# Performance work log

Hardware: AMD Instinct MI355X
Metric: run time of the kernel (lower is better)

## Reference

```python
import jax, jax.numpy as jnp
import numpy as np

DIM = 512
CHUNK = 64
DEPTH = 2
LR = 0.1
MOM = 0.9
DEC = 0.01
EPS_RMS = 1.1920929e-07  # torch.finfo(float32).eps, RMSNorm default
EPS_L2 = 1e-12           # F.normalize default eps


def rmsnorm(x, g):
    return x * jax.lax.rsqrt(jnp.mean(x * x, axis=-1, keepdims=True) + EPS_RMS) * g


def l2norm(x):
    n = jnp.sqrt(jnp.sum(x * x, axis=-1, keepdims=True))
    return x / jnp.maximum(n, EPS_L2)


def mlp(ws, x):
    # MemoryMLP: Linear(no bias) stack with SiLU between layers
    h = x
    for i, W in enumerate(ws):
        h = h @ W.T
        if i < len(ws) - 1:
            h = jax.nn.silu(h)
    return h


def setup_inputs() -> dict:
    key = jax.random.key(0)
    ks = jax.random.split(key, 16)
    D = DIM
    xav = np.sqrt(6.0 / (D + D)).astype(np.float32)  # xavier_uniform for square Linear
    inp = {
        'x': jax.random.normal(ks[0], (4, 4096, D), jnp.float32),
        'M': jax.random.normal(ks[1], (4, D, D), jnp.float32),
        'mem_W': 0.02 * jax.random.normal(ks[2], (DEPTH, D, D), jnp.float32),
        'Wk': jax.random.uniform(ks[3], (D, D), jnp.float32, -xav, xav),
        'Wv': jax.random.uniform(ks[4], (D, D), jnp.float32, -xav, xav),
        'Wq': jax.random.uniform(ks[5], (D, D), jnp.float32, -xav, xav),
        'Wout': jax.random.uniform(ks[6], (D, D), jnp.float32, -xav, xav),
        'Wgd': jax.random.uniform(ks[7], (D, D), jnp.float32, -1/np.sqrt(D), 1/np.sqrt(D)),
        'bgd': jax.random.uniform(ks[8], (D,), jnp.float32, -1/np.sqrt(D), 1/np.sqrt(D)),
        'Wgl': jax.random.uniform(ks[9], (D, D), jnp.float32, -1/np.sqrt(D), 1/np.sqrt(D)),
        'bgl': jax.random.uniform(ks[10], (D,), jnp.float32, -1/np.sqrt(D), 1/np.sqrt(D)),
        'Wgm': jax.random.uniform(ks[11], (D, D), jnp.float32, -1/np.sqrt(D), 1/np.sqrt(D)),
        'bgm': jax.random.uniform(ks[12], (D,), jnp.float32, -1/np.sqrt(D), 1/np.sqrt(D)),
        'gs': jnp.ones((D,), jnp.float32),
        'gr': jnp.ones((D,), jnp.float32),
    }
    return inp


def reference(x, M, mem_W, Wk, Wv, Wq, Wout, Wgd, bgd, Wgl, bgl, Wgm, bgm, gs, gr):
    B, S, D = x.shape
    pad = (CHUNK - S % CHUNK) % CHUNK
    if pad > 0:
        x = jnp.pad(x, ((0, 0), (0, pad), (0, 0)))
    Sp = x.shape[1]
    n = Sp // CHUNK

    # data-dependent gates from chunk means, batch-averaged scalars per chunk
    cm = x.reshape(B, n, CHUNK, D).mean(axis=2)                      # [B,n,D]
    alpha = (jax.nn.sigmoid(cm @ Wgd.T + bgd).mean(-1) * DEC).mean(0)  # [n]
    theta = (jax.nn.sigmoid(cm @ Wgl.T + bgl).mean(-1) * LR).mean(0)   # [n]
    eta = (jax.nn.sigmoid(cm @ Wgm.T + bgm).mean(-1) * MOM).mean(0)    # [n]

    x_store = rmsnorm(x, gs)
    k = l2norm(jax.nn.silu(jnp.einsum('bsd,bde->bse', x_store, M) @ Wk.T))
    v = jax.nn.silu(x_store @ Wv.T)
    q = l2norm(jax.nn.silu(rmsnorm(x, gr) @ Wq.T))

    # [n, B, C, D] chunked, scan over chunk axis
    def chunked(t):
        return t.reshape(B, n, CHUNK, D).transpose(1, 0, 2, 3)
    qc, kc, vc = chunked(q), chunked(k), chunked(v)

    ws0 = tuple(mem_W[i] for i in range(DEPTH))
    mom0 = tuple(jnp.zeros_like(w) for w in ws0)

    def step(carry, xs):
        ws, mom = carry
        q_t, k_t, v_t, a, th, et = xs
        retrieved = mlp(ws, q_t)                                   # retrieve with pre-update weights
        loss_fn = lambda w: jnp.mean((mlp(w, k_t) - v_t) ** 2)      # Eq. 12
        grads = jax.grad(loss_fn)(ws)
        mom = jax.tree.map(lambda m, g: et * m - th * g, mom, grads)   # Eq. 14
        ws = jax.tree.map(lambda w, s: (1.0 - a) * w + s, ws, mom)     # Eq. 13
        return (ws, mom), retrieved

    _, retrieved = jax.lax.scan(step, (ws0, mom0), (qc, kc, vc, alpha, theta, eta))
    retrieved = retrieved.transpose(1, 0, 2, 3).reshape(B, Sp, D)[:, :S]
    return retrieved @ Wout.T
```

## Files before the change

kernel.cpp:

```cpp
#include <hip/hip_runtime.h>
#include <math.h>
#include <stdint.h>

#define D512 512
#define SC_E (2.0f / 131072.0f)

typedef __attribute__((ext_vector_type(8))) __bf16 bf16x8;
typedef __attribute__((ext_vector_type(4))) float f32x4;
#define MFMA(a,b,c) __builtin_amdgcn_mfma_f32_16x16x32_bf16(a,b,c,0,0,0)

__device__ __forceinline__ float sigmoidf_(float z){ return 1.0f/(1.0f+expf(-z)); }
__device__ __forceinline__ float siluf_(float z){ return z/(1.0f+expf(-z)); }
__device__ __forceinline__ float dsiluf_(float z){ float s=1.0f/(1.0f+expf(-z)); return s*(1.0f+z*(1.0f-s)); }

__device__ __forceinline__ unsigned short f2bf(float x){
  union { float f; unsigned u; } c; c.f = x;
  unsigned r = (c.u + 0x7fffu + ((c.u >> 16) & 1u)) >> 16;
  return (unsigned short)r;
}
__device__ __forceinline__ float bf2f(unsigned short s){
  union { unsigned u; float f; } c; c.u = ((unsigned)s) << 16; return c.f;
}
__device__ __forceinline__ void split2(float x, unsigned short& h, unsigned short& l){
  h = f2bf(x); l = f2bf(x - bf2f(h));
}
__device__ __forceinline__ bf16x8 ldf(const unsigned short* p){ return *(const bf16x8*)p; }

__device__ __forceinline__ void stc_u32(unsigned* p, unsigned v){
  __hip_atomic_store(p, v, __ATOMIC_RELAXED, __HIP_MEMORY_SCOPE_AGENT);
}
__device__ __forceinline__ void stc_u64(unsigned long long* p, unsigned long long v){
  __hip_atomic_store(p, v, __ATOMIC_RELAXED, __HIP_MEMORY_SCOPE_AGENT);
}
__device__ __forceinline__ void stc_us4(unsigned short* p, ushort4 v){
  union { ushort4 s; unsigned long long q; } u; u.s = v;
  stc_u64((unsigned long long*)p, u.q);
}
__device__ __forceinline__ void stc_pair(unsigned short* p, unsigned short v){
  unsigned ov = (unsigned)__shfl_xor((int)(unsigned)v, 1, 64);
  if (!(threadIdx.x & 1))
    stc_u32((unsigned*)p, ((unsigned)v) | (ov << 16));
}

__device__ __forceinline__ void gbar_h(unsigned* bar, int grp, bool leader, unsigned p){
  __syncthreads();
  if (threadIdx.x == 0){
    unsigned* cnt = bar + grp*64;
    unsigned* go  = bar + 512 + grp*64;
    unsigned* gl  = bar + 1024;
    __hip_atomic_fetch_add(cnt, 1u, __ATOMIC_RELAXED, __HIP_MEMORY_SCOPE_AGENT);
    if (leader){
      while (__hip_atomic_load(cnt, __ATOMIC_RELAXED, __HIP_MEMORY_SCOPE_AGENT) < 32u*p)
        __builtin_amdgcn_s_sleep(1);
      __hip_atomic_fetch_add(gl, 1u, __ATOMIC_RELAXED, __HIP_MEMORY_SCOPE_AGENT);
      while (__hip_atomic_load(gl, __ATOMIC_RELAXED, __HIP_MEMORY_SCOPE_AGENT) < 8u*p)
        __builtin_amdgcn_s_sleep(1);
      __hip_atomic_store(go, p, __ATOMIC_RELAXED, __HIP_MEMORY_SCOPE_AGENT);
    } else {
      while (__hip_atomic_load(go, __ATOMIC_RELAXED, __HIP_MEMORY_SCOPE_AGENT) < p)
        __builtin_amdgcn_s_sleep(2);
    }
  }
  __syncthreads();
  __atomic_signal_fence(__ATOMIC_ACQUIRE);
}

template<int KTOT>
__device__ __forceinline__ void tile_ss(const unsigned short* __restrict__ A, int lda,
                                        const unsigned short* __restrict__ B, int ldb,
                                        f32x4* acc){
  const int lane = threadIdx.x & 63, wave = threadIdx.x >> 6;
  const int kq = (lane >> 4) << 3;
  const size_t aoff = (size_t)(wave*16 + (lane & 15)) * lda + kq;
  const size_t boff0 = (size_t)(lane & 15) * ldb + kq;
#pragma unroll
  for (int k0 = 0; k0 < KTOT; k0 += 32){
    bf16x8 av = ldf(A + aoff + k0);
#pragma unroll
    for (int nn = 0; nn < 4; nn++){
      bf16x8 bv = ldf(B + boff0 + (size_t)(nn*16)*ldb + k0);
      acc[nn] = MFMA(av, bv, acc[nn]);
    }
  }
}

template<int KTOT>
__device__ __forceinline__ void tile_dd(const unsigned short* __restrict__ Ah, const unsigned short* __restrict__ Al, int lda,
                                        const unsigned short* __restrict__ Bh, const unsigned short* __restrict__ Bl, int ldb,
                                        f32x4* acc){
  const int lane = threadIdx.x & 63, wave = threadIdx.x >> 6;
  const int kq = (lane >> 4) << 3;
  const size_t aoff = (size_t)(wave*16 + (lane & 15)) * lda + kq;
  const size_t boff0 = (size_t)(lane & 15) * ldb + kq;
#pragma unroll
  for (int k0 = 0; k0 < KTOT; k0 += 32){
    bf16x8 ah = ldf(Ah + aoff + k0);
    bf16x8 al = ldf(Al + aoff + k0);
#pragma unroll
    for (int nn = 0; nn < 4; nn++){
      const size_t bo = boff0 + (size_t)(nn*16)*ldb + k0;
      bf16x8 bh = ldf(Bh + bo);
      bf16x8 bl = ldf(Bl + bo);
      acc[nn] = MFMA(ah, bh, acc[nn]);
      acc[nn] = MFMA(ah, bl, acc[nn]);
      acc[nn] = MFMA(al, bh, acc[nn]);
    }
  }
}

template<int KTOT>
__device__ __forceinline__ void slice_ss(const unsigned short* __restrict__ A16, int lda,
                                         const unsigned short* __restrict__ B64, int ldb,
                                         f32x4& acc){
  const int lane = threadIdx.x & 63, wave = threadIdx.x >> 6;
  const int kq = (lane >> 4) << 3;
  const size_t aoff = (size_t)(lane & 15) * lda + kq;
  const size_t boff = (size_t)(wave*16 + (lane & 15)) * ldb + kq;
#pragma unroll
  for (int k0 = 0; k0 < KTOT; k0 += 32){
    bf16x8 av = ldf(A16 + aoff + k0);
    bf16x8 bv = ldf(B64 + boff + k0);
    acc = MFMA(av, bv, acc);
  }
}

template<int KTOT>
__device__ __forceinline__ void slice_dd(const unsigned short* __restrict__ Ah, const unsigned short* __restrict__ Al, int lda,
                                         const unsigned short* __restrict__ Bh, const unsigned short* __restrict__ Bl, int ldb,
                                         f32x4& acc){
  const int lane = threadIdx.x & 63, wave = threadIdx.x >> 6;
  const int kq = (lane >> 4) << 3;
  const size_t aoff = (size_t)(lane & 15) * lda + kq;
  const size_t boff = (size_t)(wave*16 + (lane & 15)) * ldb + kq;
#pragma unroll
  for (int k0 = 0; k0 < KTOT; k0 += 32){
    bf16x8 ah = ldf(Ah + aoff + k0);
    bf16x8 al = ldf(Al + aoff + k0);
    bf16x8 bh = ldf(Bh + boff + k0);
    bf16x8 bl = ldf(Bl + boff + k0);
    acc = MFMA(ah, bh, acc);
    acc = MFMA(ah, bl, acc);
    acc = MFMA(al, bh, acc);
  }
}

__global__ void rms_store_kernel(const float* __restrict__ x, const float* __restrict__ g,
                                 unsigned short* __restrict__ dstH){
  const size_t row = blockIdx.x; const int tid = threadIdx.x;
  const float4 xv = *(const float4*)(x + row * D512 + tid * 4);
  float ss = xv.x*xv.x + xv.y*xv.y + xv.z*xv.z + xv.w*xv.w;
  for (int o = 32; o > 0; o >>= 1) ss += __shfl_xor(ss, o, 64);
  __shared__ float w2[2];
  if ((tid & 63) == 0) w2[tid >> 6] = ss;
  __syncthreads();
  const float r = rsqrtf((w2[0] + w2[1]) * (1.0f / 512.0f) + 1.1920929e-07f);
  const float4 gv = *(const float4*)(g + tid * 4);
  ushort4 h;
  h.x = f2bf(xv.x*r*gv.x); h.y = f2bf(xv.y*r*gv.y); h.z = f2bf(xv.z*r*gv.z); h.w = f2bf(xv.w*r*gv.w);
  *(ushort4*)(dstH + row * D512 + tid * 4) = h;
}

__global__ void rms_retr_kernel(const float* __restrict__ x, const float* __restrict__ g,
                                unsigned short* __restrict__ dstH, unsigned short* __restrict__ dstL){
  const size_t row = blockIdx.x; const int tid = threadIdx.x;
  const float4 xv = *(const float4*)(x + row * D512 + tid * 4);
  float ss = xv.x*xv.x + xv.y*xv.y + xv.z*xv.z + xv.w*xv.w;
  for (int o = 32; o > 0; o >>= 1) ss += __shfl_xor(ss, o, 64);
  __shared__ float w2[2];
  if ((tid & 63) == 0) w2[tid >> 6] = ss;
  __syncthreads();
  const float r = rsqrtf((w2[0] + w2[1]) * (1.0f / 512.0f) + 1.1920929e-07f);
  const float4 gv = *(const float4*)(g + tid * 4);
  float v0 = xv.x*r*gv.x, v1 = xv.y*r*gv.y, v2 = xv.z*r*gv.z, v3 = xv.w*r*gv.w;
  ushort4 h, l;
  split2(v0, h.x, l.x); split2(v1, h.y, l.y); split2(v2, h.z, l.z); split2(v3, h.w, l.w);
  *(ushort4*)(dstH + row * D512 + tid * 4) = h;
  *(ushort4*)(dstL + row * D512 + tid * 4) = l;
}

__global__ void l2norm_split_kernel(float* __restrict__ buf,
                                    unsigned short* __restrict__ dstH, unsigned short* __restrict__ dstL){
  const size_t row = blockIdx.x; const int tid = threadIdx.x;
  float4 xv = *(const float4*)(buf + row * D512 + tid * 4);
  float ss = xv.x*xv.x + xv.y*xv.y + xv.z*xv.z + xv.w*xv.w;
  for (int o = 32; o > 0; o >>= 1) ss += __shfl_xor(ss, o, 64);
  __shared__ float w2[2];
  if ((tid & 63) == 0) w2[tid >> 6] = ss;
  __syncthreads();
  const float n = sqrtf(w2[0] + w2[1]);
  const float sc = 1.0f / fmaxf(n, 1e-12f);
  xv.x *= sc; xv.y *= sc; xv.z *= sc; xv.w *= sc;
  *(float4*)(buf + row * D512 + tid * 4) = xv;
  ushort4 h; h.x = f2bf(xv.x); h.y = f2bf(xv.y); h.z = f2bf(xv.z); h.w = f2bf(xv.w);
  *(ushort4*)(dstH + row * D512 + tid * 4) = h;
  if (dstL){
    ushort4 l;
    l.x = f2bf(xv.x - bf2f(h.x)); l.y = f2bf(xv.y - bf2f(h.y));
    l.z = f2bf(xv.z - bf2f(h.z)); l.w = f2bf(xv.w - bf2f(h.w));
    *(ushort4*)(dstL + row * D512 + tid * 4) = l;
  }
}

__global__ void cast_kernel(const float* __restrict__ src, unsigned short* __restrict__ dstH,
                            unsigned short* __restrict__ dstL, int n){
  int i = (blockIdx.x * 256 + threadIdx.x) * 4;
  if (i >= n) return;
  float4 v = *(const float4*)(src + i);
  ushort4 h; h.x = f2bf(v.x); h.y = f2bf(v.y); h.z = f2bf(v.z); h.w = f2bf(v.w);
  *(ushort4*)(dstH + i) = h;
  if (dstL){
    ushort4 l;
    l.x = f2bf(v.x - bf2f(h.x)); l.y = f2bf(v.y - bf2f(h.y));
    l.z = f2bf(v.z - bf2f(h.z)); l.w = f2bf(v.w - bf2f(h.w));
    *(ushort4*)(dstL + i) = l;
  }
}

__global__ void trans_cast_kernel(const float* __restrict__ src, unsigned short* __restrict__ dstH,
                                  unsigned short* __restrict__ dstL, int R, int C,
                                  size_t sbs, size_t dbs){
  __shared__ float t[64][65];
  const int b = blockIdx.z;
  const float* s = src + (size_t)b * sbs;
  const int r0 = blockIdx.y * 64, c0 = blockIdx.x * 64;
  for (int i = threadIdx.x; i < 4096; i += 256){
    int rr = i >> 6, cc = i & 63;
    t[rr][cc] = s[(size_t)(r0 + rr) * C + c0 + cc];
  }
  __syncthreads();
  for (int i = threadIdx.x; i < 4096; i += 256){
    int cc = i >> 6, rr = i & 63;
    float v = t[rr][cc];
    size_t off = (size_t)b * dbs + (size_t)(c0 + cc) * R + r0 + rr;
    unsigned short h = f2bf(v);
    dstH[off] = h;
    if (dstL) dstL[off] = f2bf(v - bf2f(h));
  }
}

__global__ void chunk_mean_kernel(const float* __restrict__ x, float* __restrict__ cm){
  const int c = blockIdx.x, b = blockIdx.y, tid = threadIdx.x;
  const float* base = x + ((size_t)b * 4096 + (size_t)c * 64) * D512 + tid * 4;
  float4 s = {0,0,0,0};
  for (int r = 0; r < 64; r++){
    const float4 v = *(const float4*)(base + (size_t)r * D512);
    s.x += v.x; s.y += v.y; s.z += v.z; s.w += v.w;
  }
  const float inv = 1.0f / 64.0f;
  s.x *= inv; s.y *= inv; s.z *= inv; s.w *= inv;
  *(float4*)(cm + ((size_t)b * 64 + c) * D512 + tid * 4) = s;
}

__global__ void gates_kernel(const float* __restrict__ cm,
                             const float* __restrict__ Wgd, const float* __restrict__ bgd,
                             const float* __restrict__ Wgl, const float* __restrict__ bgl,
                             const float* __restrict__ Wgm, const float* __restrict__ bgm,
                             float* __restrict__ alpha, float* __restrict__ theta, float* __restrict__ eta){
  const int c = blockIdx.x, tid = threadIdx.x;
  __shared__ float cmsh[512];
  float s0 = 0.f, s1 = 0.f, s2 = 0.f;
  for (int b = 0; b < 4; b++){
    __syncthreads();
    if (tid < 128){
      const float4 v = *(const float4*)(cm + ((size_t)b * 64 + c) * D512 + tid * 4);
      *(float4*)&cmsh[tid * 4] = v;
    }
    __syncthreads();
    for (int j = tid; j < 512; j += 256){
      float d0 = bgd[j], d1 = bgl[j], d2 = bgm[j];
      const float* w0 = Wgd + (size_t)j * D512;
      const float* w1 = Wgl + (size_t)j * D512;
      const float* w2 = Wgm + (size_t)j * D512;
      for (int kk = 0; kk < 512; kk += 4){
        const float4 cv = *(const float4*)&cmsh[kk];
        const float4 a = *(const float4*)(w0 + kk); d0 += cv.x*a.x + cv.y*a.y + cv.z*a.z + cv.w*a.w;
        const float4 e = *(const float4*)(w1 + kk); d1 += cv.x*e.x + cv.y*e.y + cv.z*e.z + cv.w*e.w;
        const float4 g = *(const float4*)(w2 + kk); d2 += cv.x*g.x + cv.y*g.y + cv.z*g.z + cv.w*g.w;
      }
      s0 += sigmoidf_(d0); s1 += sigmoidf_(d1); s2 += sigmoidf_(d2);
    }
  }
  __shared__ float red[256];
  const float inv = 1.0f / 2048.0f;
  red[tid] = s0; __syncthreads();
  for (int o = 128; o > 0; o >>= 1){ if (tid < o) red[tid] += red[tid + o]; __syncthreads(); }
  if (tid == 0) alpha[c] = red[0] * inv * 0.01f;
  __syncthreads();
  red[tid] = s1; __syncthreads();
  for (int o = 128; o > 0; o >>= 1){ if (tid < o) red[tid] += red[tid + o]; __syncthreads(); }
  if (tid == 0) theta[c] = red[0] * inv * 0.1f;
  __syncthreads();
  red[tid] = s2; __syncthreads();
  for (int o = 128; o > 0; o >>= 1){ if (tid < o) red[tid] += red[tid + o]; __syncthreads(); }
  if (tid == 0) eta[c] = red[0] * inv * 0.9f;
}

template<int MODE>
__global__ __launch_bounds__(256) void gemm_ss(const unsigned short* __restrict__ A,
                                               const unsigned short* __restrict__ B, size_t bzs,
                                               void* __restrict__ out){
  const int lane = threadIdx.x & 63, wave = threadIdx.x >> 6;
  const int er = wave*16 + ((lane >> 4) << 2), ec = lane & 15;
  const size_t row0 = (size_t)blockIdx.z * 4096 + (size_t)blockIdx.x * 64;
  const int n0 = blockIdx.y * 64;
  f32x4 acc[4] = {};
  tile_ss<512>(A + row0 * D512, D512, B + (size_t)blockIdx.z * bzs + (size_t)n0 * D512, D512, acc);
#pragma unroll
  for (int nn = 0; nn < 4; nn++)
#pragma unroll
    for (int r = 0; r < 4; r++){
      const size_t off = (row0 + er + r) * D512 + n0 + nn*16 + ec;
      float val = acc[nn][r];
      if (MODE == 0) ((unsigned short*)out)[off] = f2bf(val);
      else if (MODE == 1) ((float*)out)[off] = siluf_(val);
      else ((float*)out)[off] = val;
    }
}

template<int MODE>
__global__ __launch_bounds__(256) void gemm_dd(const unsigned short* __restrict__ Ah, const unsigned short* __restrict__ Al,
                                               const unsigned short* __restrict__ Bh, const unsigned short* __restrict__ Bl,
                                               float* __restrict__ out){
  const int lane = threadIdx.x & 63, wave = threadIdx.x >> 6;
  const int er = wave*16 + ((lane >> 4) << 2), ec = lane & 15;
  const size_t row0 = (size_t)blockIdx.x * 64;
  const int n0 = blockIdx.y * 64;
  f32x4 acc[4] = {};
  tile_dd<512>(Ah + row0 * D512, Al + row0 * D512, D512,
               Bh + (size_t)n0 * D512, Bl + (size_t)n0 * D512, D512, acc);
#pragma unroll
  for (int nn = 0; nn < 4; nn++)
#pragma unroll
    for (int r = 0; r < 4; r++){
      const size_t off = (row0 + er + r) * D512 + n0 + nn*16 + ec;
      out[off] = (MODE == 1) ? siluf_(acc[nn][r]) : acc[nn][r];
    }
}

struct ScanArgs {
  const unsigned short* kbH;
  const unsigned short* qbH; const unsigned short* qbL;
  unsigned short* W0bH; unsigned short* W0bL;
  unsigned short* hkbH; unsigned short* hkTbH;
  unsigned short* hqbH; unsigned short* hqbL;
  unsigned short* W1bH; unsigned short* W1bL;
  const float* v;
  unsigned short* ebH; unsigned short* eTbH;
  unsigned short* retH; unsigned short* retL;
  unsigned short* W1TbH; unsigned short* dpTbH;
  const float* alpha; const float* theta; const float* eta;
  const unsigned short* kTbH;
  const float* W0f; const float* W1f;
  unsigned* bar;
};

__global__ __launch_bounds__(256, 2) void scan_fused(ScanArgs P){
  const int bid = blockIdx.x;
  const int s = bid >> 6;
  const int T = bid & 63;
  const int grp = bid & 7;
  const bool leader = (bid < 8);
  const int lane = threadIdx.x & 63, wave = threadIdx.x >> 6;
  const int ar = (lane >> 4) << 2;
  const int bc = wave*16 + (lane & 15);
  const int kq = (lane >> 4) << 3;

  const int jx = T >> 3, dx = T & 7;
  f32x4 w0r = {}, m0r = {}, w1r = {}, m1r = {};
  const size_t woff = (size_t)(jx*64 + s*16 + ar) * D512 + dx*64 + bc;
#pragma unroll
  for (int r = 0; r < 4; r++){
    w0r[r] = P.W0f[woff + (size_t)r * D512];
    w1r[r] = P.W1f[woff + (size_t)r * D512];
  }

  unsigned p = 0;
  for (int t = 0; t < 64; ++t){
    float4 sp = {0,0,0,0};

    if (T < 32){
      const int ib = T >> 3, jxa = T & 7;
      f32x4 acc = {};
      slice_ss<512>(P.kbH + ((size_t)ib*4096 + (size_t)t*64 + s*16) * D512, D512,
                    P.W0bH + (size_t)jxa*64 * D512, D512, acc);
      const int i0 = ib*64 + s*16 + ar;
      const int j  = jxa*64 + bc;
      ushort4 hv;
#pragma unroll
      for (int r = 0; r < 4; r++){
        const float pfull = acc[r];
        const unsigned short hb = f2bf(siluf_(pfull));
        stc_pair(&P.hkbH[(size_t)(i0 + r) * D512 + j], hb);
        ((unsigned short*)&hv)[r] = hb;
        ((float*)&sp)[r] = dsiluf_(pfull);
      }
      stc_us4(&P.hkTbH[(size_t)j * 256 + i0], hv);
    } else {
      const int u = T - 32, bt = u >> 3, nx = u & 7;
      const size_t ab = ((size_t)bt*4096 + (size_t)t*64 + s*16) * D512;
      f32x4 acc = {};
      slice_dd<512>(P.qbH + ab, P.qbL + ab, D512,
                    P.W0bH + (size_t)nx*64 * D512, P.W0bL + (size_t)nx*64 * D512, D512, acc);
      const int i0 = bt*64 + s*16 + ar;
      const int j  = nx*64 + bc;
#pragma unroll
      for (int r = 0; r < 4; r++){
        const float h = siluf_(acc[r]);
        unsigned short hh, ll; split2(h, hh, ll);
        stc_pair(&P.hqbH[(size_t)(i0 + r) * D512 + j], hh);
        stc_pair(&P.hqbL[(size_t)(i0 + r) * D512 + j], ll);
      }
    }
    ++p; gbar_h(P.bar, grp, leader, p);

    if (T < 32){
      const int ib = T >> 3, nx = T & 7;
      f32x4 acc = {};
      slice_ss<512>(P.hkbH + (size_t)(ib*64 + s*16) * D512, D512,
                    P.W1bH + (size_t)nx*64 * D512, D512, acc);
      const int i0 = ib*64 + s*16 + ar;
      const int m  = nx*64 + bc;
      ushort4 ev;
#pragma unroll
      for (int r = 0; r < 4; r++){
        const size_t grow = (size_t)ib*4096 + (size_t)t*64 + s*16 + ar + r;
        const float vv = P.v[grow * D512 + m];
        const unsigned short eb = f2bf((acc[r] - vv) * SC_E);
        stc_pair(&P.ebH[(size_t)(i0 + r) * D512 + m], eb);
        ((unsigned short*)&ev)[r] = eb;
      }
      stc_us4(&P.eTbH[(size_t)m * 256 + i0], ev);
    } else {
      const int u = T - 32, bt = u >> 3, nx = u & 7;
      const size_t ab = (size_t)(bt*64 + s*16) * D512;
      f32x4 acc = {};
      slice_dd<512>(P.hqbH + ab, P.hqbL + ab, D512,
                    P.W1bH + (size_t)nx*64 * D512, P.W1bL + (size_t)nx*64 * D512, D512, acc);
#pragma unroll
      for (int r = 0; r < 4; r++){
        const size_t grow = (size_t)bt*4096 + (size_t)t*64 + s*16 + ar + r;
        unsigned short hh, ll; split2(acc[r], hh, ll);
        const size_t off = grow * D512 + nx*64 + bc;
        P.retH[off] = hh; P.retL[off] = ll;
      }
    }
    ++p; gbar_h(P.bar, grp, leader, p);

    if (T < 32){
      const int ib = T >> 3, jxa = T & 7;
      f32x4 acc = {};
      slice_ss<512>(P.ebH + (size_t)(ib*64 + s*16) * D512, D512,
                    P.W1TbH + (size_t)jxa*64 * D512, D512, acc);
      const int i0 = ib*64 + s*16 + ar;
      const int j  = jxa*64 + bc;
      ushort4 dv;
#pragma unroll
      for (int r = 0; r < 4; r++)
        ((unsigned short*)&dv)[r] = f2bf(acc[r] * ((const float*)&sp)[r]);
      stc_us4(&P.dpTbH[(size_t)j * 256 + i0], dv);
    }
    ++p; gbar_h(P.bar, grp, leader, p);

    {
      f32x4 g0 = {};
      const unsigned short* A16 = P.dpTbH + (size_t)(jx*64 + s*16) * 256;
      const size_t aoff = (size_t)(lane & 15) * 256 + kq;
      const size_t brow = (size_t)(dx*64 + bc) * 4096;
#pragma unroll
      for (int k0 = 0; k0 < 256; k0 += 32){
        bf16x8 av = ldf(A16 + aoff + k0);
        const int pl = k0 >> 6;
        bf16x8 bv = ldf(P.kTbH + (size_t)pl * (512*4096) + brow + (size_t)t*64 + (k0 & 63) + kq);
        g0 = MFMA(av, bv, g0);
      }
      f32x4 g1 = {};
      slice_ss<256>(P.eTbH + (size_t)(jx*64 + s*16) * 256, 256,
                    P.hkTbH + (size_t)(dx*64) * 256, 256, g1);
      const float al = P.alpha[t], th = P.theta[t], et = P.eta[t];
      ushort4 tv;
#pragma unroll
      for (int r = 0; r < 4; r++){
        const size_t off = woff + (size_t)r * D512;
        m0r[r] = et * m0r[r] - th * g0[r];
        w0r[r] = (1.0f - al) * w0r[r] + m0r[r];
        unsigned short hh, ll; split2(w0r[r], hh, ll);
        stc_pair(&P.W0bH[off], hh); stc_pair(&P.W0bL[off], ll);
        m1r[r] = et * m1r[r] - th * g1[r];
        w1r[r] = (1.0f - al) * w1r[r] + m1r[r];
        unsigned short h1, l1; split2(w1r[r], h1, l1);
        stc_pair(&P.W1bH[off], h1); stc_pair(&P.W1bL[off], l1);
        ((unsigned short*)&tv)[r] = h1;
      }
      stc_us4(&P.W1TbH[(size_t)(dx*64 + bc) * D512 + jx*64 + s*16 + ar], tv);
    }
    ++p; gbar_h(P.bar, grp, leader, p);

    __builtin_amdgcn_fence(__ATOMIC_ACQUIRE, "agent");
  }
}

extern "C" void kernel_launch(void* const* d_in, const int* in_sizes, int n_in,
                              void* d_out, int out_size, void* d_ws, size_t ws_size,
                              hipStream_t stream) {
  const float* x    = (const float*)d_in[0];
  const float* Mb   = (const float*)d_in[1];
  const float* memW = (const float*)d_in[2];
  const float* Wk   = (const float*)d_in[3];
  const float* Wv   = (const float*)d_in[4];
  const float* Wq   = (const float*)d_in[5];
  const float* Wout = (const float*)d_in[6];
  const float* Wgd  = (const float*)d_in[7];
  const float* bgd  = (const float*)d_in[8];
  const float* Wgl  = (const float*)d_in[9];
  const float* bgl  = (const float*)d_in[10];
  const float* Wgm  = (const float*)d_in[11];
  const float* bgm  = (const float*)d_in[12];
  const float* gs   = (const float*)d_in[13];
  const float* gr   = (const float*)d_in[14];
  float* out = (float*)d_out;

  const size_t NBIG = (size_t)4 * 4096 * 512;
  char* p = (char*)d_ws;
  auto alloc_f = [&](size_t n) -> float* {
    p = (char*)(((uintptr_t)p + 255) & ~(uintptr_t)255);
    float* r = (float*)p; p += n * 4; return r;
  };
  auto alloc_s = [&](size_t n) -> unsigned short* {
    p = (char*)(((uintptr_t)p + 255) & ~(uintptr_t)255);
    unsigned short* r = (unsigned short*)p; p += n * 2; return r;
  };

  float* v       = alloc_f(NBIG);
  float* scratch = alloc_f(NBIG);
  float* W0f     = alloc_f(262144);
  float* W1f     = alloc_f(262144);
  float* cm      = alloc_f(131072);
  float* alpha   = alloc_f(64);
  float* theta   = alloc_f(64);
  float* eta     = alloc_f(64);
  unsigned* bar  = (unsigned*)alloc_f(2048);

  unsigned short* xsbH = alloc_s(NBIG);
  unsigned short* xmbH = alloc_s(NBIG);
  unsigned short* xrbL = alloc_s(NBIG);
  unsigned short* qbH  = alloc_s(NBIG);
  unsigned short* qbL  = alloc_s(NBIG);
  unsigned short* kbH  = alloc_s(NBIG);
  unsigned short* kTbH = alloc_s(NBIG);
  unsigned short* W0bH = alloc_s(262144);
  unsigned short* W0bL = alloc_s(262144);
  unsigned short* W1bH = alloc_s(262144);
  unsigned short* W1bL = alloc_s(262144);
  unsigned short* W1TbH = alloc_s(262144);
  unsigned short* WkbH = alloc_s(262144);
  unsigned short* WvbH = alloc_s(262144);
  unsigned short* WqbH = alloc_s(262144);
  unsigned short* WqbL = alloc_s(262144);
  unsigned short* WoutbH = alloc_s(262144);
  unsigned short* WoutbL = alloc_s(262144);
  unsigned short* MTbH = alloc_s((size_t)4 * 262144);
  unsigned short* hkbH = alloc_s(131072);
  unsigned short* hkTbH = alloc_s(131072);
  unsigned short* hqbH = alloc_s(131072);
  unsigned short* hqbL = alloc_s(131072);
  unsigned short* ebH  = alloc_s(131072);
  unsigned short* eTbH = alloc_s(131072);
  unsigned short* dpTbH = alloc_s(131072);

  hipMemcpyAsync(W0f, memW, 2 * 262144 * sizeof(float), hipMemcpyDeviceToDevice, stream);
  hipMemsetAsync(bar, 0, 2048 * sizeof(unsigned), stream);
  cast_kernel<<<256, 256, 0, stream>>>(memW, W0bH, W0bL, 262144);
  cast_kernel<<<256, 256, 0, stream>>>(memW + 262144, W1bH, W1bL, 262144);
  trans_cast_kernel<<<dim3(8, 8, 1), 256, 0, stream>>>(memW + 262144, W1TbH, nullptr, 512, 512, 0, 0);
  cast_kernel<<<256, 256, 0, stream>>>(Wk, WkbH, nullptr, 262144);
  cast_kernel<<<256, 256, 0, stream>>>(Wv, WvbH, nullptr, 262144);
  cast_kernel<<<256, 256, 0, stream>>>(Wq, WqbH, WqbL, 262144);
  cast_kernel<<<256, 256, 0, stream>>>(Wout, WoutbH, WoutbL, 262144);
  trans_cast_kernel<<<dim3(8, 8, 4), 256, 0, stream>>>(Mb, MTbH, nullptr, 512, 512, 262144, 262144);

  rms_store_kernel<<<16384, 128, 0, stream>>>(x, gs, xsbH);
  chunk_mean_kernel<<<dim3(64, 4), 128, 0, stream>>>(x, cm);
  gates_kernel<<<64, 256, 0, stream>>>(cm, Wgd, bgd, Wgl, bgl, Wgm, bgm, alpha, theta, eta);

  gemm_ss<0><<<dim3(64, 8, 4), 256, 0, stream>>>(xsbH, MTbH, 262144, xmbH);
  gemm_ss<1><<<dim3(256, 8, 1), 256, 0, stream>>>(xmbH, WkbH, 0, scratch);
  l2norm_split_kernel<<<16384, 128, 0, stream>>>(scratch, kbH, nullptr);
  trans_cast_kernel<<<dim3(8, 64, 4), 256, 0, stream>>>(scratch, kTbH, nullptr, 4096, 512, 2097152, 2097152);
  gemm_ss<1><<<dim3(256, 8, 1), 256, 0, stream>>>(xsbH, WvbH, 0, v);
  rms_retr_kernel<<<16384, 128, 0, stream>>>(x, gr, xmbH, xrbL);
  gemm_dd<1><<<dim3(256, 8), 256, 0, stream>>>(xmbH, xrbL, WqbH, WqbL, scratch);
  l2norm_split_kernel<<<16384, 128, 0, stream>>>(scratch, qbH, qbL);

  unsigned short* retH = xsbH;
  unsigned short* retL = xmbH;

  ScanArgs sa;
  sa.kbH = kbH; sa.qbH = qbH; sa.qbL = qbL;
  sa.W0bH = W0bH; sa.W0bL = W0bL;
  sa.hkbH = hkbH; sa.hkTbH = hkTbH;
  sa.hqbH = hqbH; sa.hqbL = hqbL;
  sa.W1bH = W1bH; sa.W1bL = W1bL;
  sa.v = v;
  sa.ebH = ebH; sa.eTbH = eTbH;
  sa.retH = retH; sa.retL = retL;
  sa.W1TbH = W1TbH; sa.dpTbH = dpTbH;
  sa.alpha = alpha; sa.theta = theta; sa.eta = eta;
  sa.kTbH = kTbH;
  sa.W0f = W0f; sa.W1f = W1f;
  sa.bar = bar;
  scan_fused<<<256, 256, 0, stream>>>(sa);

  gemm_dd<2><<<dim3(256, 8), 256, 0, stream>>>(retH, retL, WoutbH, WoutbL, out);
}
```

Before: 3.591 ms.

## Split scan GEMM K-dimension across two wave halves and batch gate dot products

The persistent scan kernel now launches 512 threads per block. Two wave groups each compute half of the K reduction for every slice GEMM and combine the partial sums through shared memory, and the two weight-gradient GEMMs in the update phase are assigned to separate wave halves. This shortens the serial MFMA chain per wave on the latency-bound chunk scan, at the cost of extra __syncthreads, LDS traffic and lower occupancy per CU. Separately, the gates kernel loads all four batch chunk-means at once and reuses each weight row load across the four batches.

```diff
diff --git a/kernel.cpp b/kernel.cpp
--- a/kernel.cpp
+++ b/kernel.cpp
@@ -111,11 +111,11 @@
 template<int KTOT>
 __device__ __forceinline__ void slice_ss(const unsigned short* __restrict__ A16, int lda,
                                          const unsigned short* __restrict__ B64, int ldb,
-                                         f32x4& acc){
-  const int lane = threadIdx.x & 63, wave = threadIdx.x >> 6;
-  const int kq = (lane >> 4) << 3;
+                                         f32x4& acc, int koff){
+  const int lane = threadIdx.x & 63, w4 = (threadIdx.x >> 6) & 3;
+  const int kq = ((lane >> 4) << 3) + koff;
   const size_t aoff = (size_t)(lane & 15) * lda + kq;
-  const size_t boff = (size_t)(wave*16 + (lane & 15)) * ldb + kq;
+  const size_t boff = (size_t)(w4*16 + (lane & 15)) * ldb + kq;
 #pragma unroll
   for (int k0 = 0; k0 < KTOT; k0 += 32){
     bf16x8 av = ldf(A16 + aoff + k0);
@@ -127,11 +127,11 @@
 template<int KTOT>
 __device__ __forceinline__ void slice_dd(const unsigned short* __restrict__ Ah, const unsigned short* __restrict__ Al, int lda,
                                          const unsigned short* __restrict__ Bh, const unsigned short* __restrict__ Bl, int ldb,
-                                         f32x4& acc){
-  const int lane = threadIdx.x & 63, wave = threadIdx.x >> 6;
-  const int kq = (lane >> 4) << 3;
+                                         f32x4& acc, int koff){
+  const int lane = threadIdx.x & 63, w4 = (threadIdx.x >> 6) & 3;
+  const int kq = ((lane >> 4) << 3) + koff;
   const size_t aoff = (size_t)(lane & 15) * lda + kq;
-  const size_t boff = (size_t)(wave*16 + (lane & 15)) * ldb + kq;
+  const size_t boff = (size_t)(w4*16 + (lane & 15)) * ldb + kq;
 #pragma unroll
   for (int k0 = 0; k0 < KTOT; k0 += 32){
     bf16x8 ah = ldf(Ah + aoff + k0);
@@ -257,27 +257,35 @@
                              const float* __restrict__ Wgm, const float* __restrict__ bgm,
                              float* __restrict__ alpha, float* __restrict__ theta, float* __restrict__ eta){
   const int c = blockIdx.x, tid = threadIdx.x;
-  __shared__ float cmsh[512];
+  __shared__ float cmsh[4][512];
+#pragma unroll
+  for (int b = 0; b < 4; b++)
+    if (tid < 128)
+      *(float4*)&cmsh[b][tid * 4] = *(const float4*)(cm + ((size_t)b * 64 + c) * D512 + tid * 4);
+  __syncthreads();
   float s0 = 0.f, s1 = 0.f, s2 = 0.f;
-  for (int b = 0; b < 4; b++){
-    __syncthreads();
-    if (tid < 128){
-      const float4 v = *(const float4*)(cm + ((size_t)b * 64 + c) * D512 + tid * 4);
-      *(float4*)&cmsh[tid * 4] = v;
-    }
-    __syncthreads();
-    for (int j = tid; j < 512; j += 256){
-      float d0 = bgd[j], d1 = bgl[j], d2 = bgm[j];
-      const float* w0 = Wgd + (size_t)j * D512;
-      const float* w1 = Wgl + (size_t)j * D512;
-      const float* w2 = Wgm + (size_t)j * D512;
-      for (int kk = 0; kk < 512; kk += 4){
-        const float4 cv = *(const float4*)&cmsh[kk];
-        const float4 a = *(const float4*)(w0 + kk); d0 += cv.x*a.x + cv.y*a.y + cv.z*a.z + cv.w*a.w;
-        const float4 e = *(const float4*)(w1 + kk); d1 += cv.x*e.x + cv.y*e.y + cv.z*e.z + cv.w*e.w;
-        const float4 g = *(const float4*)(w2 + kk); d2 += cv.x*g.x + cv.y*g.y + cv.z*g.z + cv.w*g.w;
-      }
-      s0 += sigmoidf_(d0); s1 += sigmoidf_(d1); s2 += sigmoidf_(d2);
+  for (int j = tid; j < 512; j += 256){
+    float d0[4], d1[4], d2[4];
+#pragma unroll
+    for (int b = 0; b < 4; b++){ d0[b] = bgd[j]; d1[b] = bgl[j]; d2[b] = bgm[j]; }
+    const float* w0 = Wgd + (size_t)j * D512;
+    const float* w1 = Wgl + (size_t)j * D512;
+    const float* w2 = Wgm + (size_t)j * D512;
+    for (int kk = 0; kk < 512; kk += 4){
+      const float4 a = *(const float4*)(w0 + kk);
+      const float4 e = *(const float4*)(w1 + kk);
+      const float4 g = *(const float4*)(w2 + kk);
+#pragma unroll
+      for (int b = 0; b < 4; b++){
+        const float4 cv = *(const float4*)&cmsh[b][kk];
+        d0[b] += cv.x*a.x + cv.y*a.y + cv.z*a.z + cv.w*a.w;
+        d1[b] += cv.x*e.x + cv.y*e.y + cv.z*e.z + cv.w*e.w;
+        d2[b] += cv.x*g.x + cv.y*g.y + cv.z*g.z + cv.w*g.w;
+      }
+    }
+#pragma unroll
+    for (int b = 0; b < 4; b++){
+      s0 += sigmoidf_(d0[b]); s1 += sigmoidf_(d1[b]); s2 += sigmoidf_(d2[b]);
     }
   }
   __shared__ float red[256];
@@ -354,24 +362,33 @@
   unsigned* bar;
 };
 
-__global__ __launch_bounds__(256, 2) void scan_fused(ScanArgs P){
+__global__ __launch_bounds__(512, 1) void scan_fused(ScanArgs P){
   const int bid = blockIdx.x;
   const int s = bid >> 6;
   const int T = bid & 63;
   const int grp = bid & 7;
   const bool leader = (bid < 8);
-  const int lane = threadIdx.x & 63, wave = threadIdx.x >> 6;
+  const int tid = threadIdx.x;
+  const int lane = tid & 63;
+  const int wave = tid >> 6;
+  const int w4 = wave & 3;
+  const int h = wave >> 2;
   const int ar = (lane >> 4) << 2;
-  const int bc = wave*16 + (lane & 15);
+  const int bc = w4*16 + (lane & 15);
   const int kq = (lane >> 4) << 3;
+  const int koff = h * 256;
+
+  __shared__ f32x4 red[4][64];
 
   const int jx = T >> 3, dx = T & 7;
   f32x4 w0r = {}, m0r = {}, w1r = {}, m1r = {};
   const size_t woff = (size_t)(jx*64 + s*16 + ar) * D512 + dx*64 + bc;
-#pragma unroll
-  for (int r = 0; r < 4; r++){
-    w0r[r] = P.W0f[woff + (size_t)r * D512];
-    w1r[r] = P.W1f[woff + (size_t)r * D512];
+  if (h == 0){
+#pragma unroll
+    for (int r = 0; r < 4; r++){
+      w0r[r] = P.W0f[woff + (size_t)r * D512];
+      w1r[r] = P.W1f[woff + (size_t)r * D512];
+    }
   }
 
   unsigned p = 0;
@@ -381,34 +398,44 @@
     if (T < 32){
       const int ib = T >> 3, jxa = T & 7;
       f32x4 acc = {};
-      slice_ss<512>(P.kbH + ((size_t)ib*4096 + (size_t)t*64 + s*16) * D512, D512,
-                    P.W0bH + (size_t)jxa*64 * D512, D512, acc);
-      const int i0 = ib*64 + s*16 + ar;
-      const int j  = jxa*64 + bc;
-      ushort4 hv;
-#pragma unroll
-      for (int r = 0; r < 4; r++){
-        const float pfull = acc[r];
-        const unsigned short hb = f2bf(siluf_(pfull));
-        stc_pair(&P.hkbH[(size_t)(i0 + r) * D512 + j], hb);
-        ((unsigned short*)&hv)[r] = hb;
-        ((float*)&sp)[r] = dsiluf_(pfull);
-      }
-      stc_us4(&P.hkTbH[(size_t)j * 256 + i0], hv);
+      slice_ss<256>(P.kbH + ((size_t)ib*4096 + (size_t)t*64 + s*16) * D512, D512,
+                    P.W0bH + (size_t)jxa*64 * D512, D512, acc, koff);
+      if (h == 1) red[w4][lane] = acc;
+      __syncthreads();
+      if (h == 0){
+        const f32x4 o = red[w4][lane];
+        const int i0 = ib*64 + s*16 + ar;
+        const int j  = jxa*64 + bc;
+        ushort4 hv;
+#pragma unroll
+        for (int r = 0; r < 4; r++){
+          const float pfull = acc[r] + o[r];
+          const unsigned short hb = f2bf(siluf_(pfull));
+          stc_pair(&P.hkbH[(size_t)(i0 + r) * D512 + j], hb);
+          ((unsigned short*)&hv)[r] = hb;
+          ((float*)&sp)[r] = dsiluf_(pfull);
+        }
+        stc_us4(&P.hkTbH[(size_t)j * 256 + i0], hv);
+      }
     } else {
       const int u = T - 32, bt = u >> 3, nx = u & 7;
       const size_t ab = ((size_t)bt*4096 + (size_t)t*64 + s*16) * D512;
       f32x4 acc = {};
-      slice_dd<512>(P.qbH + ab, P.qbL + ab, D512,
-                    P.W0bH + (size_t)nx*64 * D512, P.W0bL + (size_t)nx*64 * D512, D512, acc);
-      const int i0 = bt*64 + s*16 + ar;
-      const int j  = nx*64 + bc;
-#pragma unroll
-      for (int r = 0; r < 4; r++){
-        const float h = siluf_(acc[r]);
-        unsigned short hh, ll; split2(h, hh, ll);
-        stc_pair(&P.hqbH[(size_t)(i0 + r) * D512 + j], hh);
-        stc_pair(&P.hqbL[(size_t)(i0 + r) * D512 + j], ll);
+      slice_dd<256>(P.qbH + ab, P.qbL + ab, D512,
+                    P.W0bH + (size_t)nx*64 * D512, P.W0bL + (size_t)nx*64 * D512, D512, acc, koff);
+      if (h == 1) red[w4][lane] = acc;
+      __syncthreads();
+      if (h == 0){
+        const f32x4 o = red[w4][lane];
+        const int i0 = bt*64 + s*16 + ar;
+        const int j  = nx*64 + bc;
+#pragma unroll
+        for (int r = 0; r < 4; r++){
+          const float hq = siluf_(acc[r] + o[r]);
+          unsigned short hh, ll; split2(hq, hh, ll);
+          stc_pair(&P.hqbH[(size_t)(i0 + r) * D512 + j], hh);
+          stc_pair(&P.hqbL[(size_t)(i0 + r) * D512 + j], ll);
+        }
       }
     }
     ++p; gbar_h(P.bar, grp, leader, p);
@@ -416,32 +443,42 @@
     if (T < 32){
       const int ib = T >> 3, nx = T & 7;
       f32x4 acc = {};
-      slice_ss<512>(P.hkbH + (size_t)(ib*64 + s*16) * D512, D512,
-                    P.W1bH + (size_t)nx*64 * D512, D512, acc);
-      const int i0 = ib*64 + s*16 + ar;
-      const int m  = nx*64 + bc;
-      ushort4 ev;
-#pragma unroll
-      for (int r = 0; r < 4; r++){
-        const size_t grow = (size_t)ib*4096 + (size_t)t*64 + s*16 + ar + r;
-        const float vv = P.v[grow * D512 + m];
-        const unsigned short eb = f2bf((acc[r] - vv) * SC_E);
-        stc_pair(&P.ebH[(size_t)(i0 + r) * D512 + m], eb);
-        ((unsigned short*)&ev)[r] = eb;
-      }
-      stc_us4(&P.eTbH[(size_t)m * 256 + i0], ev);
+      slice_ss<256>(P.hkbH + (size_t)(ib*64 + s*16) * D512, D512,
+                    P.W1bH + (size_t)nx*64 * D512, D512, acc, koff);
+      if (h == 1) red[w4][lane] = acc;
+      __syncthreads();
+      if (h == 0){
+        const f32x4 o = red[w4][lane];
+        const int i0 = ib*64 + s*16 + ar;
+        const int m  = nx*64 + bc;
+        ushort4 ev;
+#pragma unroll
+        for (int r = 0; r < 4; r++){
+          const size_t grow = (size_t)ib*4096 + (size_t)t*64 + s*16 + ar + r;
+          const float vv = P.v[grow * D512 + m];
+          const unsigned short eb = f2bf((acc[r] + o[r] - vv) * SC_E);
+          stc_pair(&P.ebH[(size_t)(i0 + r) * D512 + m], eb);
+          ((unsigned short*)&ev)[r] = eb;
+        }
+        stc_us4(&P.eTbH[(size_t)m * 256 + i0], ev);
+      }
     } else {
       const int u = T - 32, bt = u >> 3, nx = u & 7;
       const size_t ab = (size_t)(bt*64 + s*16) * D512;
       f32x4 acc = {};
-      slice_dd<512>(P.hqbH + ab, P.hqbL + ab, D512,
-                    P.W1bH + (size_t)nx*64 * D512, P.W1bL + (size_t)nx*64 * D512, D512, acc);
-#pragma unroll
-      for (int r = 0; r < 4; r++){
-        const size_t grow = (size_t)bt*4096 + (size_t)t*64 + s*16 + ar + r;
-        unsigned short hh, ll; split2(acc[r], hh, ll);
-        const size_t off = grow * D512 + nx*64 + bc;
-        P.retH[off] = hh; P.retL[off] = ll;
+      slice_dd<256>(P.hqbH + ab, P.hqbL + ab, D512,
+                    P.W1bH + (size_t)nx*64 * D512, P.W1bL + (size_t)nx*64 * D512, D512, acc, koff);
+      if (h == 1) red[w4][lane] = acc;
+      __syncthreads();
+      if (h == 0){
+        const f32x4 o = red[w4][lane];
+#pragma unroll
+        for (int r = 0; r < 4; r++){
+          const size_t grow = (size_t)bt*4096 + (size_t)t*64 + s*16 + ar + r;
+          unsigned short hh, ll; split2(acc[r] + o[r], hh, ll);
+          const size_t off = grow * D512 + nx*64 + bc;
+          P.retH[off] = hh; P.retL[off] = ll;
+        }
       }
     }
     ++p; gbar_h(P.bar, grp, leader, p);
@@ -449,49 +486,61 @@
     if (T < 32){
       const int ib = T >> 3, jxa = T & 7;
       f32x4 acc = {};
-      slice_ss<512>(P.ebH + (size_t)(ib*64 + s*16) * D512, D512,
-                    P.W1TbH + (size_t)jxa*64 * D512, D512, acc);
-      const int i0 = ib*64 + s*16 + ar;
-      const int j  = jxa*64 + bc;
-      ushort4 dv;
-#pragma unroll
-      for (int r = 0; r < 4; r++)
-        ((unsigned short*)&dv)[r] = f2bf(acc[r] * ((const float*)&sp)[r]);
-      stc_us4(&P.dpTbH[(size_t)j * 256 + i0], dv);
+      slice_ss<256>(P.ebH + (size_t)(ib*64 + s*16) * D512, D512,
+                    P.W1TbH + (size_t)jxa*64 * D512, D512, acc, koff);
+      if (h == 1) red[w4][lane] = acc;
+      __syncthreads();
+      if (h == 0){
+        const f32x4 o = red[w4][lane];
+        const int i0 = ib*64 + s*16 + ar;
+        const int j  = jxa*64 + bc;
+        ushort4 dv;
+#pragma unroll
+        for (int r = 0; r < 4; r++)
+          ((unsigned short*)&dv)[r] = f2bf((acc[r] + o[r]) * ((const float*)&sp)[r]);
+        stc_us4(&P.dpTbH[(size_t)j * 256 + i0], dv);
+      }
     }
     ++p; gbar_h(P.bar, grp, leader, p);
 
     {
-      f32x4 g0 = {};
-      const unsigned short* A16 = P.dpTbH + (size_t)(jx*64 + s*16) * 256;
-      const size_t aoff = (size_t)(lane & 15) * 256 + kq;
-      const size_t brow = (size_t)(dx*64 + bc) * 4096;
-#pragma unroll
-      for (int k0 = 0; k0 < 256; k0 += 32){
-        bf16x8 av = ldf(A16 + aoff + k0);
-        const int pl = k0 >> 6;
-        bf16x8 bv = ldf(P.kTbH + (size_t)pl * (512*4096) + brow + (size_t)t*64 + (k0 & 63) + kq);
-        g0 = MFMA(av, bv, g0);
-      }
-      f32x4 g1 = {};
-      slice_ss<256>(P.eTbH + (size_t)(jx*64 + s*16) * 256, 256,
-                    P.hkTbH + (size_t)(dx*64) * 256, 256, g1);
-      const float al = P.alpha[t], th = P.theta[t], et = P.eta[t];
-      ushort4 tv;
-#pragma unroll
-      for (int r = 0; r < 4; r++){
-        const size_t off = woff + (size_t)r * D512;
-        m0r[r] = et * m0r[r] - th * g0[r];
-        w0r[r] = (1.0f - al) * w0r[r] + m0r[r];
-        unsigned short hh, ll; split2(w0r[r], hh, ll);
-        stc_pair(&P.W0bH[off], hh); stc_pair(&P.W0bL[off], ll);
-        m1r[r] = et * m1r[r] - th * g1[r];
-        w1r[r] = (1.0f - al) * w1r[r] + m1r[r];
-        unsigned short h1, l1; split2(w1r[r], h1, l1);
-        stc_pair(&P.W1bH[off], h1); stc_pair(&P.W1bL[off], l1);
-        ((unsigned short*)&tv)[r] = h1;
-      }
-      stc_us4(&P.W1TbH[(size_t)(dx*64 + bc) * D512 + jx*64 + s*16 + ar], tv);
+      f32x4 g = {};
+      if (h == 0){
+        const unsigned short* A16 = P.dpTbH + (size_t)(jx*64 + s*16) * 256;
+        const size_t aoff = (size_t)(lane & 15) * 256 + kq;
+        const size_t brow = (size_t)(dx*64 + bc) * 4096;
+#pragma unroll
+        for (int k0 = 0; k0 < 256; k0 += 32){
+          bf16x8 av = ldf(A16 + aoff + k0);
+          const int pl = k0 >> 6;
+          bf16x8 bv = ldf(P.kTbH + (size_t)pl * (512*4096) + brow + (size_t)t*64 + (k0 & 63) + kq);
+          g = MFMA(av, bv, g);
+        }
+      } else {
+        slice_ss<256>(P.eTbH + (size_t)(jx*64 + s*16) * 256, 256,
+                      P.hkTbH + (size_t)(dx*64) * 256, 256, g, 0);
+        red[w4][lane] = g;
+      }
+      __syncthreads();
+      if (h == 0){
+        const f32x4 g1 = red[w4][lane];
+        const float al = P.alpha[t], th = P.theta[t], et = P.eta[t];
+        ushort4 tv;
+#pragma unroll
+        for (int r = 0; r < 4; r++){
+          const size_t off = woff + (size_t)r * D512;
+          m0r[r] = et * m0r[r] - th * g[r];
+          w0r[r] = (1.0f - al) * w0r[r] + m0r[r];
+          unsigned short hh, ll; split2(w0r[r], hh, ll);
+          stc_pair(&P.W0bH[off], hh); stc_pair(&P.W0bL[off], ll);
+          m1r[r] = et * m1r[r] - th * g1[r];
+          w1r[r] = (1.0f - al) * w1r[r] + m1r[r];
+          unsigned short h1, l1; split2(w1r[r], h1, l1);
+          stc_pair(&P.W1bH[off], h1); stc_pair(&P.W1bL[off], l1);
+          ((unsigned short*)&tv)[r] = h1;
+        }
+        stc_us4(&P.W1TbH[(size_t)(dx*64 + bc) * D512 + jx*64 + s*16 + ar], tv);
+      }
     }
     ++p; gbar_h(P.bar, grp, leader, p);
 
@@ -608,7 +657,7 @@
   sa.kTbH = kTbH;
   sa.W0f = W0f; sa.W1f = W1f;
   sa.bar = bar;
-  scan_fused<<<256, 256, 0, stream>>>(sa);
+  scan_fused<<<256, 512, 0, stream>>>(sa);
 
   gemm_dd<2><<<dim3(256, 8), 256, 0, stream>>>(retH, retL, WoutbH, WoutbL, out);
 }
```

New measurement: 3.839 ms. +6.9%, slower.
